# Performance work log

Hardware: AMD Instinct MI355X
Metric: run time of the kernel (lower is better)

The kernel has to match this reference:

```python
import jax, jax.numpy as jnp
import numpy as np

N1, N2, C = 1024, 1024, 128
H = 2 * C  # h_dim = in_dim * 2


def setup_inputs() -> dict:
    key = jax.random.key(0)
    ks = jax.random.split(key, 8)
    std = 0.01
    return {
        "X": jax.random.normal(ks[0], (N1, C), dtype=jnp.float32),
        "Y": jax.random.normal(ks[1], (N2, C), dtype=jnp.float32),
        "Wsr": jax.random.normal(ks[2], (C, C), dtype=jnp.float32) * std,
        "Wtg": jax.random.normal(ks[3], (C, C), dtype=jnp.float32) * std,
        "W1": jax.random.normal(ks[4], (H, H), dtype=jnp.float32) * std,
        "b1": jnp.zeros((H,), dtype=jnp.float32),
        "W2": jax.random.normal(ks[5], (1, H), dtype=jnp.float32) * std,
        "b2": jnp.zeros((1,), dtype=jnp.float32),
    }


def reference(X, Y, Wsr, Wtg, W1, b1, W2, b2):
    # project_sr / project_tg (bias-free Linear: x @ W^T)
    Xp = X @ Wsr.T  # [N1, C]
    Yp = Y @ Wtg.T  # [N2, C]
    # First fc_M linear on concat([X_k, Y_k]) == split-weight form:
    # concat(x, y) @ W1^T = x @ W1[:, :C]^T + y @ W1[:, C:]^T
    Xh = Xp @ W1[:, :C].T  # [N1, 2C]
    Yh = Yp @ W1[:, C:].T  # [N2, 2C]
    Hid = jax.nn.relu(Xh[:, None, :] + Yh[None, :, :] + b1)  # [N1, N2, 2C]
    # Second linear 2C -> 1, then squeeze
    M = jnp.einsum('abh,h->ab', Hid, W2[0]) + b2[0]  # [N1, N2]
    return M
```

## Files before the change

### kernel.cpp

```cpp
#include <hip/hip_runtime.h>

#define N1 1024
#define N2 1024
#define CDIM 128
#define HDIM 256


__global__ __launch_bounds__(256) void fold_weights(
    const float* __restrict__ W1, const float* __restrict__ Wsr,
    const float* __restrict__ Wtg, float* __restrict__ Wx,
    float* __restrict__ Wy) {
  int id = blockIdx.x * 256 + threadIdx.x;
  int m  = id / (HDIM * CDIM);
  int r  = id % (HDIM * CDIM);
  int h  = r / CDIM;
  int j  = r % CDIM;
  const float* Wm    = m ? Wtg : Wsr;
  const float* w1row = W1 + (size_t)h * HDIM + (m ? CDIM : 0);
  float acc = 0.f;
#pragma unroll 8
  for (int c = 0; c < CDIM; ++c)
    acc = fmaf(w1row[c], Wm[(size_t)c * CDIM + j], acc);
  (m ? Wy : Wx)[(size_t)h * CDIM + j] = acc;
}

__global__ __launch_bounds__(256) void gemm_ht(
    const float* __restrict__ X, const float* __restrict__ Y,
    const float* __restrict__ Wx, const float* __restrict__ Wy,
    const float* __restrict__ b1, float* __restrict__ XhT,
    float* __restrict__ YhT) {
  const float* A = blockIdx.z ? Y : X;
  const float* W = blockIdx.z ? Wy : Wx;
  float*       O = blockIdx.z ? YhT : XhT;
  const bool useBias = (blockIdx.z == 0);

  __shared__ float Al[64][132];
  __shared__ float Wl[128][68];

  const int t  = threadIdx.x;
  const int n0 = blockIdx.x * 64;
  const int h0 = blockIdx.y * 64;

#pragma unroll
  for (int it = 0; it < 8; ++it) {
    int row = it * 8 + (t >> 5);
    int col = (t & 31) * 4;
    *(float4*)(&Al[row][col]) =
        *(const float4*)(&A[(size_t)(n0 + row) * CDIM + col]);
  }
#pragma unroll
  for (int it = 0; it < 8; ++it) {
    int h = it * 8 + (t >> 5);
    int k = (t & 31) * 4;
    float4 w = *(const float4*)(&W[(size_t)(h0 + h) * CDIM + k]);
    Wl[k + 0][h] = w.x;
    Wl[k + 1][h] = w.y;
    Wl[k + 2][h] = w.z;
    Wl[k + 3][h] = w.w;
  }
  __syncthreads();

  const int tx = t & 15;
  const int ty = t >> 4;
  float acc[4][4];
#pragma unroll
  for (int i = 0; i < 4; ++i)
#pragma unroll
    for (int j = 0; j < 4; ++j) acc[i][j] = 0.f;

  for (int k4 = 0; k4 < CDIM; k4 += 4) {
    float a_[4][4];
#pragma unroll
    for (int i = 0; i < 4; ++i) {
      float4 v = *(const float4*)(&Al[ty * 4 + i][k4]);
      a_[i][0] = v.x; a_[i][1] = v.y; a_[i][2] = v.z; a_[i][3] = v.w;
    }
#pragma unroll
    for (int kk = 0; kk < 4; ++kk) {
      float4 w = *(const float4*)(&Wl[k4 + kk][tx * 4]);
      float wj[4] = {w.x, w.y, w.z, w.w};
#pragma unroll
      for (int i = 0; i < 4; ++i)
#pragma unroll
        for (int j = 0; j < 4; ++j)
          acc[i][j] = fmaf(a_[i][kk], wj[j], acc[i][j]);
    }
  }

#pragma unroll
  for (int j = 0; j < 4; ++j) {
    int h = h0 + tx * 4 + j;
    float b = useBias ? b1[h] : 0.f;
    float4 v = {acc[0][j] + b, acc[1][j] + b, acc[2][j] + b, acc[3][j] + b};
    *(float4*)(&O[(size_t)h * N1 + n0 + ty * 4]) = v;
  }
}

__global__ __launch_bounds__(256) void uv_reduce(
    const float* __restrict__ XhT, const float* __restrict__ YhT,
    const float* __restrict__ W2, float* __restrict__ uv) {
  int tid = blockIdx.x * 256 + threadIdx.x;
  const float* T = (tid < N1) ? XhT : YhT;
  int n = tid & (N1 - 1);
  float acc = 0.f;
#pragma unroll 8
  for (int h = 0; h < HDIM; ++h)
    acc = fmaf(T[(size_t)h * N1 + n], W2[h], acc);
  uv[tid] = 0.5f * acc;
}

__global__ __launch_bounds__(256, 4) void pairwise_abs(
    const float* __restrict__ XhT, const float* __restrict__ YhT,
    const float* __restrict__ W2, float* __restrict__ Pbase) {
  __shared__ float Xl[32][64];
  __shared__ float Yl[32][128];

  const int t  = threadIdx.x;
  const int b0 = blockIdx.x * 128;
  const int a0 = blockIdx.y * 64;
  const int hb = blockIdx.z * 32;
  float* P = Pbase + (size_t)blockIdx.z * ((size_t)N1 * N2);

#pragma unroll
  for (int it = 0; it < 2; ++it) {
    int idx = it * 256 + t;
    int hl  = idx >> 4;
    int c4  = (idx & 15) * 4;
    *(float4*)(&Xl[hl][c4]) =
        *(const float4*)(&XhT[(size_t)(hb + hl) * N1 + a0 + c4]);
  }
#pragma unroll
  for (int it = 0; it < 4; ++it) {
    int idx = it * 256 + t;
    int hl  = idx >> 5;
    int c   = idx & 31;
    int pos = (c >> 1) | ((c & 1) << 4);
    *(float4*)(&Yl[hl][pos * 4]) =
        *(const float4*)(&YhT[(size_t)(hb + hl) * N2 + b0 + c * 4]);
  }
  __syncthreads();

  const int tx = t & 15;
  const int ty = t >> 4;

  float acc[4][8];
#pragma unroll
  for (int i = 0; i < 4; ++i)
#pragma unroll
    for (int j = 0; j < 8; ++j) acc[i][j] = 0.f;

  for (int h4 = 0; h4 < 32; h4 += 4) {
    const float4 w4 = *(const float4*)(&W2[hb + h4]);
    const float wh[4] = {0.5f * w4.x, 0.5f * w4.y, 0.5f * w4.z, 0.5f * w4.w};
#pragma unroll
    for (int hh = 0; hh < 4; ++hh) {
      const int h = h4 + hh;
      float4 xv  = *(const float4*)(&Xl[h][ty * 4]);
      float4 yv0 = *(const float4*)(&Yl[h][tx * 4]);
      float4 yv1 = *(const float4*)(&Yl[h][64 + tx * 4]);
      const float xa[4] = {xv.x, xv.y, xv.z, xv.w};
      const float yb[8] = {yv0.x, yv0.y, yv0.z, yv0.w,
                           yv1.x, yv1.y, yv1.z, yv1.w};
      const float w = wh[hh];
#pragma unroll
      for (int i = 0; i < 4; ++i) {
#pragma unroll
        for (int j = 0; j < 8; j += 2) {
          float s0 = xa[i] + yb[j];
          float s1 = xa[i] + yb[j + 1];
          acc[i][j]     = fmaf(__builtin_fabsf(s0), w, acc[i][j]);
          acc[i][j + 1] = fmaf(__builtin_fabsf(s1), w, acc[i][j + 1]);
        }
      }
    }
  }

#pragma unroll
  for (int i = 0; i < 4; ++i) {
    int a = a0 + ty * 4 + i;
    float4 v0 = {acc[i][0], acc[i][1], acc[i][2], acc[i][3]};
    float4 v1 = {acc[i][4], acc[i][5], acc[i][6], acc[i][7]};
    *(float4*)(&P[(size_t)a * N2 + b0 + tx * 8])     = v0;
    *(float4*)(&P[(size_t)a * N2 + b0 + tx * 8 + 4]) = v1;
  }
}

__global__ __launch_bounds__(256) void finalize(
    const float* __restrict__ P, const float* __restrict__ uv,
    const float* __restrict__ b2, float* __restrict__ out) {
  int i4 = blockIdx.x * 256 + threadIdx.x;
  int a  = i4 >> 8;
  int c4 = i4 & 255;
  float4 s = ((const float4*)P)[i4];
#pragma unroll
  for (int z = 1; z < 8; ++z) {
    float4 p = ((const float4*)(P + (size_t)z * N1 * N2))[i4];
    s.x += p.x; s.y += p.y; s.z += p.z; s.w += p.w;
  }
  const float ua = uv[a] + b2[0];
  float4 vb = ((const float4*)(uv + N1))[c4];
  float4 o = {s.x + ua + vb.x, s.y + ua + vb.y, s.z + ua + vb.z,
              s.w + ua + vb.w};
  ((float4*)out)[i4] = o;
}

extern "C" void kernel_launch(void* const* d_in, const int* in_sizes, int n_in,
                              void* d_out, int out_size, void* d_ws,
                              size_t ws_size, hipStream_t stream) {
  const float* X   = (const float*)d_in[0];
  const float* Y   = (const float*)d_in[1];
  const float* Wsr = (const float*)d_in[2];
  const float* Wtg = (const float*)d_in[3];
  const float* W1  = (const float*)d_in[4];
  const float* b1  = (const float*)d_in[5];
  const float* W2  = (const float*)d_in[6];
  const float* b2  = (const float*)d_in[7];
  float* out = (float*)d_out;

  float* ws  = (float*)d_ws;
  float* Wx  = ws;
  float* Wy  = ws + 32768;
  float* XhT = ws + 65536;
  float* YhT = ws + 65536 + 262144;
  float* uv  = ws + 589824;
  float* P   = ws + 591872;

  fold_weights<<<256, 256, 0, stream>>>(W1, Wsr, Wtg, Wx, Wy);
  gemm_ht<<<dim3(16, 4, 2), 256, 0, stream>>>(X, Y, Wx, Wy, b1, XhT, YhT);
  uv_reduce<<<8, 256, 0, stream>>>(XhT, YhT, W2, uv);
  pairwise_abs<<<dim3(8, 16, 8), 256, 0, stream>>>(XhT, YhT, W2, P);
  finalize<<<1024, 256, 0, stream>>>(P, uv, b2, out);
}
```

Before: 135.2 us.

## Fuse uv reduction into projection GEMM epilogue and swizzle shared-memory tiles

The separate uv_reduce kernel is removed. Its per-row dot product with W2 is now computed in the gemm_ht epilogue, combined with wavefront shuffles and added to uv with atomicAdd, and fold_weights zeroes uv first. The GEMM shared tiles switch to float4 row-major layouts with an XOR swizzle, so W no longer needs a transposed scalar store and the inner loop reads float4 along k. This saves one launch and one pass over XhT/YhT, at the cost of atomics, which make the accumulation order nondeterministic.

```diff
diff --git a/kernel.cpp b/kernel.cpp
--- a/kernel.cpp
+++ b/kernel.cpp
@@ -9,8 +9,9 @@
 __global__ __launch_bounds__(256) void fold_weights(
     const float* __restrict__ W1, const float* __restrict__ Wsr,
     const float* __restrict__ Wtg, float* __restrict__ Wx,
-    float* __restrict__ Wy) {
+    float* __restrict__ Wy, float* __restrict__ uv) {
   int id = blockIdx.x * 256 + threadIdx.x;
+  if (id < 2048) uv[id] = 0.f;
   int m  = id / (HDIM * CDIM);
   int r  = id % (HDIM * CDIM);
   int h  = r / CDIM;
@@ -27,15 +28,16 @@
 __global__ __launch_bounds__(256) void gemm_ht(
     const float* __restrict__ X, const float* __restrict__ Y,
     const float* __restrict__ Wx, const float* __restrict__ Wy,
-    const float* __restrict__ b1, float* __restrict__ XhT,
-    float* __restrict__ YhT) {
+    const float* __restrict__ b1, const float* __restrict__ W2,
+    float* __restrict__ XhT, float* __restrict__ YhT,
+    float* __restrict__ uv) {
   const float* A = blockIdx.z ? Y : X;
   const float* W = blockIdx.z ? Wy : Wx;
   float*       O = blockIdx.z ? YhT : XhT;
   const bool useBias = (blockIdx.z == 0);
 
-  __shared__ float Al[64][132];
-  __shared__ float Wl[128][68];
+  __shared__ float4 Al4[64 * 32];
+  __shared__ float4 Wl4[64 * 32];
 
   const int t  = threadIdx.x;
   const int n0 = blockIdx.x * 64;
@@ -43,70 +45,87 @@
 
 #pragma unroll
   for (int it = 0; it < 8; ++it) {
-    int row = it * 8 + (t >> 5);
-    int col = (t & 31) * 4;
-    *(float4*)(&Al[row][col]) =
-        *(const float4*)(&A[(size_t)(n0 + row) * CDIM + col]);
-  }
-#pragma unroll
-  for (int it = 0; it < 8; ++it) {
-    int h = it * 8 + (t >> 5);
-    int k = (t & 31) * 4;
-    float4 w = *(const float4*)(&W[(size_t)(h0 + h) * CDIM + k]);
-    Wl[k + 0][h] = w.x;
-    Wl[k + 1][h] = w.y;
-    Wl[k + 2][h] = w.z;
-    Wl[k + 3][h] = w.w;
+    int idx = it * 256 + t;
+    int row = idx >> 5;
+    int c   = idx & 31;
+    int slot = c ^ (((row >> 3) & 7) << 2);
+    Al4[row * 32 + slot] =
+        *(const float4*)(&A[(size_t)(n0 + row) * CDIM + c * 4]);
+    Wl4[row * 32 + slot] =
+        *(const float4*)(&W[(size_t)(h0 + row) * CDIM + c * 4]);
   }
   __syncthreads();
 
   const int tx = t & 15;
   const int ty = t >> 4;
+
+  int aBase[4], aSwz[4], wBase[4], wSwz[4];
+#pragma unroll
+  for (int i = 0; i < 4; ++i) {
+    int rA = ty * 4 + i;
+    aBase[i] = rA * 32;
+    aSwz[i]  = ((rA >> 3) & 7) << 2;
+    int rW = tx * 4 + i;
+    wBase[i] = rW * 32;
+    wSwz[i]  = ((rW >> 3) & 7) << 2;
+  }
+
   float acc[4][4];
 #pragma unroll
   for (int i = 0; i < 4; ++i)
 #pragma unroll
     for (int j = 0; j < 4; ++j) acc[i][j] = 0.f;
 
-  for (int k4 = 0; k4 < CDIM; k4 += 4) {
-    float a_[4][4];
+  for (int q = 0; q < 32; ++q) {
+    float4 av[4], wv[4];
+#pragma unroll
+    for (int i = 0; i < 4; ++i) av[i] = Al4[aBase[i] + (q ^ aSwz[i])];
+#pragma unroll
+    for (int j = 0; j < 4; ++j) wv[j] = Wl4[wBase[j] + (q ^ wSwz[j])];
 #pragma unroll
     for (int i = 0; i < 4; ++i) {
-      float4 v = *(const float4*)(&Al[ty * 4 + i][k4]);
-      a_[i][0] = v.x; a_[i][1] = v.y; a_[i][2] = v.z; a_[i][3] = v.w;
+      const float ai[4] = {av[i].x, av[i].y, av[i].z, av[i].w};
+#pragma unroll
+      for (int j = 0; j < 4; ++j) {
+        acc[i][j] = fmaf(ai[0], wv[j].x, acc[i][j]);
+        acc[i][j] = fmaf(ai[1], wv[j].y, acc[i][j]);
+        acc[i][j] = fmaf(ai[2], wv[j].z, acc[i][j]);
+        acc[i][j] = fmaf(ai[3], wv[j].w, acc[i][j]);
+      }
     }
-#pragma unroll
-    for (int kk = 0; kk < 4; ++kk) {
-      float4 w = *(const float4*)(&Wl[k4 + kk][tx * 4]);
-      float wj[4] = {w.x, w.y, w.z, w.w};
-#pragma unroll
-      for (int i = 0; i < 4; ++i)
-#pragma unroll
-        for (int j = 0; j < 4; ++j)
-          acc[i][j] = fmaf(a_[i][kk], wj[j], acc[i][j]);
-    }
-  }
-
+  }
+
+  float4 bj4 = useBias ? *(const float4*)(&b1[h0 + tx * 4])
+                       : float4{0.f, 0.f, 0.f, 0.f};
+  const float bj[4] = {bj4.x, bj4.y, bj4.z, bj4.w};
+  float4 w24 = *(const float4*)(&W2[h0 + tx * 4]);
+  const float hw[4] = {0.5f * w24.x, 0.5f * w24.y, 0.5f * w24.z, 0.5f * w24.w};
+
+  float pu[4];
+#pragma unroll
+  for (int i = 0; i < 4; ++i) {
+    float val[4];
+#pragma unroll
+    for (int j = 0; j < 4; ++j) val[j] = acc[i][j] + bj[j];
+    pu[i] = val[0] * hw[0] + val[1] * hw[1] + val[2] * hw[2] + val[3] * hw[3];
+    acc[i][0] = val[0]; acc[i][1] = val[1]; acc[i][2] = val[2]; acc[i][3] = val[3];
+  }
 #pragma unroll
   for (int j = 0; j < 4; ++j) {
     int h = h0 + tx * 4 + j;
-    float b = useBias ? b1[h] : 0.f;
-    float4 v = {acc[0][j] + b, acc[1][j] + b, acc[2][j] + b, acc[3][j] + b};
+    float4 v = {acc[0][j], acc[1][j], acc[2][j], acc[3][j]};
     *(float4*)(&O[(size_t)h * N1 + n0 + ty * 4]) = v;
   }
-}
-
-__global__ __launch_bounds__(256) void uv_reduce(
-    const float* __restrict__ XhT, const float* __restrict__ YhT,
-    const float* __restrict__ W2, float* __restrict__ uv) {
-  int tid = blockIdx.x * 256 + threadIdx.x;
-  const float* T = (tid < N1) ? XhT : YhT;
-  int n = tid & (N1 - 1);
-  float acc = 0.f;
-#pragma unroll 8
-  for (int h = 0; h < HDIM; ++h)
-    acc = fmaf(T[(size_t)h * N1 + n], W2[h], acc);
-  uv[tid] = 0.5f * acc;
+#pragma unroll
+  for (int i = 0; i < 4; ++i) {
+    float p = pu[i];
+    p += __shfl_xor(p, 1);
+    p += __shfl_xor(p, 2);
+    p += __shfl_xor(p, 4);
+    p += __shfl_xor(p, 8);
+    if (tx == 0)
+      atomicAdd(&uv[blockIdx.z * N1 + n0 + ty * 4 + i], p);
+  }
 }
 
 __global__ __launch_bounds__(256, 4) void pairwise_abs(
@@ -225,9 +244,9 @@
   float* uv  = ws + 589824;
   float* P   = ws + 591872;
 
-  fold_weights<<<256, 256, 0, stream>>>(W1, Wsr, Wtg, Wx, Wy);
-  gemm_ht<<<dim3(16, 4, 2), 256, 0, stream>>>(X, Y, Wx, Wy, b1, XhT, YhT);
-  uv_reduce<<<8, 256, 0, stream>>>(XhT, YhT, W2, uv);
+  fold_weights<<<256, 256, 0, stream>>>(W1, Wsr, Wtg, Wx, Wy, uv);
+  gemm_ht<<<dim3(16, 4, 2), 256, 0, stream>>>(X, Y, Wx, Wy, b1, W2,
+                                              XhT, YhT, uv);
   pairwise_abs<<<dim3(8, 16, 8), 256, 0, stream>>>(XhT, YhT, W2, P);
   finalize<<<1024, 256, 0, stream>>>(P, uv, b2, out);
 }
```

New measurement: 121.7 us. 10.0% less time.
